# Optimization experiments

Hardware: AMD Instinct MI355X
Metric: run time of the kernel (lower is better)

The kernel has to match this reference:

```python
import jax, jax.numpy as jnp
import numpy as np

B, T, D, H = 4, 2048, 1024, 16
HD = D // H  # head dim = 64


def setup_inputs() -> dict:
    key = jax.random.key(0)
    ks = jax.random.split(key, 6)
    s = 0.02
    return {
        "x": jax.random.normal(ks[0], (B, T, D), dtype=jnp.float32),
        "Wk": jax.random.normal(ks[1], (D, D), dtype=jnp.float32) * s,
        "Wq": jax.random.normal(ks[2], (D, D), dtype=jnp.float32) * s,
        "Wv": jax.random.normal(ks[3], (D, D), dtype=jnp.float32) * s,
        "Wp": jax.random.normal(ks[4], (D, D), dtype=jnp.float32) * s,
        "bp": jnp.zeros((D,), dtype=jnp.float32),
    }


def reference(x, Wk, Wq, Wv, Wp, bp):
    # nn.Linear applies x @ W.T; weights here are stored torch-style [out, in]
    Bq, Tq, _ = x.shape
    k = (x @ Wk.T).reshape(Bq, Tq, H, HD).transpose(0, 2, 1, 3)  # [B,H,T,hd]
    q = (x @ Wq.T).reshape(Bq, Tq, H, HD).transpose(0, 2, 1, 3)
    v = (x @ Wv.T).reshape(Bq, Tq, H, HD).transpose(0, 2, 1, 3)
    scale = HD ** -0.5
    attn = jnp.einsum('bhqd,bhkd->bhqk', q, k) * scale  # [B,H,T,T]
    causal = jnp.tril(jnp.ones((Tq, Tq), dtype=bool))
    attn = jnp.where(causal, attn, -jnp.inf)
    attn = jax.nn.softmax(attn, axis=-1)
    # dropout p=0.0 -> identity (eval semantics)
    out = jnp.einsum('bhqk,bhkd->bhqd', attn, v)  # [B,H,T,hd]
    out = out.transpose(0, 2, 1, 3).reshape(Bq, Tq, D)
    return out @ Wp.T + bp
```

## Files before the change

### kernel.cpp

```cpp
#include <hip/hip_runtime.h>
#include <hip/hip_bf16.h>
#include <stdint.h>


typedef __bf16 bf16x8 __attribute__((ext_vector_type(8)));
typedef float floatx4 __attribute__((ext_vector_type(4)));
typedef unsigned short ushort_t;
typedef unsigned short ushortx8 __attribute__((ext_vector_type(8)));
typedef unsigned short ushortx4 __attribute__((ext_vector_type(4)));
typedef short shortx4 __attribute__((ext_vector_type(4)));

#define MFMA16(a, b, c) __builtin_amdgcn_mfma_f32_16x16x32_bf16((a), (b), (c), 0, 0, 0)
#define MFMA16K16(a, b, c) __builtin_amdgcn_mfma_f32_16x16x16bf16_1k((a), (b), (c), 0, 0, 0)
#define EXP2F(x) __builtin_amdgcn_exp2f(x)

static __device__ __forceinline__ ushort_t f2bfu(float f) {
  union { float f; unsigned u; } v; v.f = f;
  unsigned r = v.u + 0x7FFFu + ((v.u >> 16) & 1u);
  return (ushort_t)(r >> 16);
}

static __device__ __forceinline__ unsigned pack_bf2(float lo, float hi) {
  return __builtin_amdgcn_perm(__float_as_uint(hi), __float_as_uint(lo), 0x07060302);
}

static __device__ __forceinline__ void gl_lds16(const void* g, void* l) {
  __builtin_amdgcn_global_load_lds(
      (const __attribute__((address_space(1))) void*)g,
      (__attribute__((address_space(3))) void*)l, 16, 0, 0);
}

__global__ void cvt_all(const float* __restrict__ x,  const float* __restrict__ wk,
                        const float* __restrict__ wq, const float* __restrict__ wv,
                        const float* __restrict__ wp, ushortx4* __restrict__ dst) {
  const int i = blockIdx.x * blockDim.x + threadIdx.x;
  const float4* src; int off;
  if (i < 2097152) { src = (const float4*)x; off = i; }
  else {
    const int r = i - 2097152;
    const int sel = r >> 18;
    off = r & 262143;
    src = (const float4*)(sel == 0 ? wk : sel == 1 ? wq : sel == 2 ? wv : wp);
  }
  const float4 f = src[off];
  ushortx4 o;
  o[0] = f2bfu(f.x); o[1] = f2bfu(f.y); o[2] = f2bfu(f.z); o[3] = f2bfu(f.w);
  dst[i] = o;
}

__global__ __launch_bounds__(512, 2) void gemm_qkv(
    const ushort_t* __restrict__ X,
    const ushort_t* __restrict__ Wq, const ushort_t* __restrict__ Wk,
    const ushort_t* __restrict__ Wv,
    ushort_t* __restrict__ qb, ushort_t* __restrict__ kb, ushort_t* __restrict__ vtb)
{
  const int L = (int)blockIdx.x;
  const int rr = L & 7, mm = L >> 3;
  const int m0 = (rr + 8 * (mm & 3)) * 256;
  const int rest = mm >> 2;
  const int n0 = (rest & 3) * 256;
  const int z = rest >> 2;

  const ushort_t* Bm = (z == 0) ? Wq : (z == 1) ? Wk : Wv;

  __shared__ ushort_t As0[256 * 64];
  __shared__ ushort_t As1[256 * 64];
  __shared__ ushort_t Bs0[256 * 64];
  __shared__ ushort_t Bs1[256 * 64];

  const int tid = threadIdx.x;
  const int w = tid >> 6, lane = tid & 63, g = lane >> 4, c = lane & 15;
  const int wm = w >> 2, wn = w & 3;
  const int cswz = c & 7;

  floatx4 acc[8][4];
  const floatx4 zero4 = {0.f, 0.f, 0.f, 0.f};
#pragma unroll
  for (int i = 0; i < 8; ++i)
#pragma unroll
    for (int j = 0; j < 4; ++j) acc[i][j] = zero4;

  const int srow = tid >> 3;
  const int gsw  = ((tid & 7) ^ (srow & 7)) * 8;

#pragma unroll
  for (int p = 0; p < 4; ++p) {
    gl_lds16(&X [(size_t)(m0 + p * 64 + srow) * 1024 + gsw], &As0[p * 4096 + tid * 8]);
    gl_lds16(&Bm[(size_t)(n0 + p * 64 + srow) * 1024 + gsw], &Bs0[p * 4096 + tid * 8]);
  }

  auto ktile = [&](const ushort_t* __restrict__ Ac, const ushort_t* __restrict__ Bc,
                   ushort_t* __restrict__ An, ushort_t* __restrict__ Bn,
                   int kn, bool stagenext) {
    if (stagenext) {
      gl_lds16(&X [(size_t)(m0 + srow) * 1024 + kn + gsw], &An[tid * 8]);
      gl_lds16(&Bm[(size_t)(n0 + srow) * 1024 + kn + gsw], &Bn[tid * 8]);
      asm volatile("s_waitcnt vmcnt(2)" ::: "memory");
    } else {
      asm volatile("s_waitcnt vmcnt(0)" ::: "memory");
    }
    __builtin_amdgcn_s_barrier();

    bf16x8 bfr[4][2];
#pragma unroll
    for (int j = 0; j < 4; ++j)
#pragma unroll
      for (int kk = 0; kk < 2; ++kk)
        bfr[j][kk] = *reinterpret_cast<const bf16x8*>(
            &Bc[(wn * 64 + j * 16 + c) * 64 + ((kk * 4 + g) ^ cswz) * 8]);

#pragma unroll
    for (int q = 0; q < 4; ++q) {
      bf16x8 af[2][2];
#pragma unroll
      for (int ii = 0; ii < 2; ++ii)
#pragma unroll
        for (int kk = 0; kk < 2; ++kk)
          af[ii][kk] = *reinterpret_cast<const bf16x8*>(
              &Ac[(wm * 128 + (q * 2 + ii) * 16 + c) * 64 + ((kk * 4 + g) ^ cswz) * 8]);
      if (q && stagenext) {
        gl_lds16(&X [(size_t)(m0 + q * 64 + srow) * 1024 + kn + gsw], &An[q * 4096 + tid * 8]);
        gl_lds16(&Bm[(size_t)(n0 + q * 64 + srow) * 1024 + kn + gsw], &Bn[q * 4096 + tid * 8]);
      }
      __builtin_amdgcn_s_setprio(1);
#pragma unroll
      for (int ii = 0; ii < 2; ++ii)
#pragma unroll
        for (int j = 0; j < 4; ++j)
#pragma unroll
          for (int kk = 0; kk < 2; ++kk)
            acc[q * 2 + ii][j] = MFMA16(af[ii][kk], bfr[j][kk], acc[q * 2 + ii][j]);
      __builtin_amdgcn_s_setprio(0);
    }
    __builtin_amdgcn_s_barrier();
  };

  for (int kt = 0; kt < 16; kt += 2) {
    ktile(As0, Bs0, As1, Bs1, (kt + 1) * 64, true);
    ktile(As1, Bs1, As0, Bs0, (kt + 2) * 64, kt < 14);
  }

#pragma unroll
  for (int i = 0; i < 8; ++i) {
#pragma unroll
    for (int j = 0; j < 4; ++j) {
      const int mbase = m0 + wm * 128 + i * 16 + g * 4;
      const int n = n0 + wn * 64 + j * 16 + c;
      const int h = n >> 6, d = n & 63;
      if (z == 2) {
        const int bb = mbase >> 11, t = mbase & 2047;
        ushortx4 pk;
#pragma unroll
        for (int r = 0; r < 4; ++r) pk[r] = f2bfu(acc[i][j][r]);
        *reinterpret_cast<ushortx4*>(&vtb[(size_t)((bb * 16 + h) * 64 + d) * 2048 + t]) = pk;
      } else {
        ushort_t* ob = (z == 0) ? qb : kb;
#pragma unroll
        for (int r = 0; r < 4; ++r) {
          const int m = mbase + r;
          const int bb = m >> 11, t = m & 2047;
          ob[(size_t)((bb * 16 + h) * 2048 + t) * 64 + d] = f2bfu(acc[i][j][r]);
        }
      }
    }
  }
}

__global__ __launch_bounds__(256, 4) void attn_kernel(
    const ushort_t* __restrict__ qbuf, const ushort_t* __restrict__ kbuf,
    const ushort_t* __restrict__ vtbuf, ushort_t* __restrict__ obuf)
{
  const int L = (int)(blockIdx.x + 16 * (blockIdx.y + 16 * blockIdx.z));
  const int rr = L & 7, mm = L >> 3;
  const int j = mm >> 3;
  const int bhl = rr * 8 + (mm & 7);
  const int h = bhl & 15, b = bhl >> 4;

  const int tid = threadIdx.x, w = tid >> 6, lane = tid & 63, g = lane >> 4, c = lane & 15;

  __shared__ ushort_t Kl[128 * 64];
  __shared__ ushort_t Vl[64 * 128];

  const size_t bh = (size_t)(b * 16 + h);
  const ushort_t* kb_bh = kbuf + bh * 2048 * 64;
  const ushort_t* vt_bh = vtbuf + bh * 64 * 2048;
  const ushort_t* qb_bh = qbuf + bh * 2048 * 64;

  const int rb0 = j * 64 + w * 16;
  const int rb1 = (31 - j) * 64 + w * 16;

  bf16x8 aq0[2], aq1[2];
  {
    const ushort_t* qp0 = qb_bh + (size_t)(rb0 + c) * 64;
    aq0[0] = *reinterpret_cast<const bf16x8*>(qp0 + g * 8);
    aq0[1] = *reinterpret_cast<const bf16x8*>(qp0 + 32 + g * 8);
    const ushort_t* qp1 = qb_bh + (size_t)(rb1 + c) * 64;
    aq1[0] = *reinterpret_cast<const bf16x8*>(qp1 + g * 8);
    aq1[1] = *reinterpret_cast<const bf16x8*>(qp1 + 32 + g * 8);
  }

  floatx4 oacc0[4], oacc1[4];
  float l0 = 0.f, l1 = 0.f;
  const floatx4 zero4 = {0.f, 0.f, 0.f, 0.f};
#pragma unroll
  for (int td = 0; td < 4; ++td) { oacc0[td] = zero4; oacc1[td] = zero4; }

  const int krow_s = tid >> 3;
  const int kgsw   = ((tid & 7) ^ (krow_s & 7)) * 8;
  const int vrow_s = tid >> 4;
  const int vgsw   = ((tid & 15) ^ (vrow_s & 15)) * 8;

  const float SCALE = 0.18033688011112042f;

  const int n128 = (33 - j) >> 1;
  for (int kt = 0; kt < n128; ++kt) {
    const int key0 = kt * 128;
#pragma unroll
    for (int p = 0; p < 4; ++p) {
      const int kr = p * 32 + krow_s;
      gl_lds16(&kb_bh[(size_t)(key0 + kr) * 64 + kgsw], &Kl[p * 2048 + tid * 8]);
      const int vr = p * 16 + vrow_s;
      gl_lds16(&vt_bh[(size_t)vr * 2048 + key0 + vgsw], &Vl[p * 2048 + tid * 8]);
    }
    __syncthreads();

#pragma unroll
    for (int s = 0; s < 2; ++s) {
      const int ti = 2 * kt + s;
      const int key0s = ti * 64;
#pragma unroll
      for (int grp = 0; grp < 2; ++grp) {
        const int lim = (grp == 0) ? j : 31 - j;
        if (ti > lim) continue;
        const int rb = (grp == 0) ? rb0 : rb1;
        const bf16x8 b0 = (grp == 0) ? aq0[0] : aq1[0];
        const bf16x8 b1 = (grp == 0) ? aq0[1] : aq1[1];

        float pv[4][4];
#pragma unroll
        for (int t4 = 0; t4 < 4; ++t4) {
          const int krow = s * 64 + t4 * 16 + c;
          const bf16x8 k0f = *reinterpret_cast<const bf16x8*>(&Kl[krow * 64 + ((g) ^ (c & 7)) * 8]);
          const bf16x8 k1f = *reinterpret_cast<const bf16x8*>(&Kl[krow * 64 + ((4 + g) ^ (c & 7)) * 8]);
          floatx4 sa = zero4;
          sa = MFMA16(k0f, b0, sa);
          sa = MFMA16(k1f, b1, sa);
          if (ti == lim) {
            const int q = rb + c;
#pragma unroll
            for (int r = 0; r < 4; ++r) {
              const int key = key0s + t4 * 16 + g * 4 + r;
              const float e = EXP2F(sa[r] * SCALE);
              pv[t4][r] = (key <= q) ? e : 0.f;
            }
          } else {
#pragma unroll
            for (int r = 0; r < 4; ++r) pv[t4][r] = EXP2F(sa[r] * SCALE);
          }
        }
        float lsum = 0.f;
#pragma unroll
        for (int t4 = 0; t4 < 4; ++t4)
          lsum += (pv[t4][0] + pv[t4][1]) + (pv[t4][2] + pv[t4][3]);
        if (grp == 0) l0 += lsum; else l1 += lsum;

#pragma unroll
        for (int t4 = 0; t4 < 4; ++t4) {
          union { unsigned u[2]; shortx4 v; } pk;
          pk.u[0] = pack_bf2(pv[t4][0], pv[t4][1]);
          pk.u[1] = pack_bf2(pv[t4][2], pv[t4][3]);
          const int cc = s * 8 + t4 * 2 + (g >> 1);
          const int ko = (g & 1) * 4;
#pragma unroll
          for (int td = 0; td < 4; ++td) {
            const shortx4 va = *reinterpret_cast<const shortx4*>(
                &Vl[(td * 16 + c) * 128 + (cc ^ c) * 8 + ko]);
            if (grp == 0) oacc0[td] = MFMA16K16(va, pk.v, oacc0[td]);
            else          oacc1[td] = MFMA16K16(va, pk.v, oacc1[td]);
          }
        }
      }
    }
    __syncthreads();
  }

#pragma unroll
  for (int grp = 0; grp < 2; ++grp) {
    float ls = (grp == 0) ? l0 : l1;
    ls += __shfl_xor(ls, 16, 64);
    ls += __shfl_xor(ls, 32, 64);
    const float inv = 1.f / ls;
    const int q = ((grp == 0) ? rb0 : rb1) + c;
    ushort_t* ob = &obuf[((size_t)(b * 2048 + q) * 16 + h) * 64];
#pragma unroll
    for (int td = 0; td < 4; ++td) {
      const floatx4 oa = (grp == 0) ? oacc0[td] : oacc1[td];
      ushortx4 pk;
#pragma unroll
      for (int r = 0; r < 4; ++r) pk[r] = f2bfu(oa[r] * inv);
      *reinterpret_cast<ushortx4*>(&ob[td * 16 + g * 4]) = pk;
    }
  }
}

__global__ __launch_bounds__(256) void gemm_proj(
    const ushort_t* __restrict__ A, const ushort_t* __restrict__ Wp,
    const float* __restrict__ bias, float* __restrict__ out)
{
  const int L = (int)(blockIdx.x + 64 * blockIdx.y);
  const int rr = L & 7, mm = L >> 3;
  const int m0 = (rr + 8 * (mm & 7)) * 128;
  const int n0 = (mm >> 3) * 128;

  __shared__ ushort_t Al[128 * 64];
  __shared__ ushort_t Bl[128 * 64];
  const int tid = threadIdx.x;
  const int w = tid >> 6, lane = tid & 63, g = lane >> 4, c = lane & 15;
  const int wm = w >> 1, wn = w & 1;
  const int cswz = c & 7;

  floatx4 acc[4][4];
  const floatx4 zero4 = {0.f, 0.f, 0.f, 0.f};
#pragma unroll
  for (int i = 0; i < 4; ++i)
#pragma unroll
    for (int j = 0; j < 4; ++j) acc[i][j] = zero4;

  const int srow = tid >> 3;
  const int gsw  = ((tid & 7) ^ (srow & 7)) * 8;

  for (int k0 = 0; k0 < 1024; k0 += 64) {
#pragma unroll
    for (int p = 0; p < 4; ++p) {
      const int row = p * 32 + srow;
      gl_lds16(&A [(size_t)(m0 + row) * 1024 + k0 + gsw], &Al[p * 2048 + tid * 8]);
      gl_lds16(&Wp[(size_t)(n0 + row) * 1024 + k0 + gsw], &Bl[p * 2048 + tid * 8]);
    }
    __syncthreads();
#pragma unroll
    for (int kk = 0; kk < 2; ++kk) {
      bf16x8 af[4], bfr[4];
#pragma unroll
      for (int i = 0; i < 4; ++i) {
        const int sw = ((kk * 4 + g) ^ cswz) * 8;
        af[i]  = *reinterpret_cast<const bf16x8*>(&Al[(wm * 64 + i * 16 + c) * 64 + sw]);
        bfr[i] = *reinterpret_cast<const bf16x8*>(&Bl[(wn * 64 + i * 16 + c) * 64 + sw]);
      }
#pragma unroll
      for (int i = 0; i < 4; ++i)
#pragma unroll
        for (int j = 0; j < 4; ++j)
          acc[i][j] = MFMA16(af[i], bfr[j], acc[i][j]);
    }
    __syncthreads();
  }

#pragma unroll
  for (int i = 0; i < 4; ++i) {
#pragma unroll
    for (int j = 0; j < 4; ++j) {
      const int n = n0 + wn * 64 + j * 16 + c;
      const float bv = bias[n];
#pragma unroll
      for (int r = 0; r < 4; ++r) {
        const int m = m0 + wm * 64 + i * 16 + g * 4 + r;
        out[(size_t)m * 1024 + n] = acc[i][j][r] + bv;
      }
    }
  }
}

extern "C" void kernel_launch(void* const* d_in, const int* in_sizes, int n_in,
                              void* d_out, int out_size, void* d_ws, size_t ws_size,
                              hipStream_t stream) {
  const float* x  = (const float*)d_in[0];
  const float* Wk = (const float*)d_in[1];
  const float* Wq = (const float*)d_in[2];
  const float* Wv = (const float*)d_in[3];
  const float* Wp = (const float*)d_in[4];
  const float* bp = (const float*)d_in[5];
  float* out = (float*)d_out;

  char* ws = (char*)d_ws;
  const size_t SZ_X = (size_t)8192 * 1024 * 2;
  const size_t SZ_W = (size_t)1024 * 1024 * 2;
  ushort_t* xb    = (ushort_t*)ws;  ws += SZ_X;
  ushort_t* wkb   = (ushort_t*)ws;  ws += SZ_W;
  ushort_t* wqb   = (ushort_t*)ws;  ws += SZ_W;
  ushort_t* wvb   = (ushort_t*)ws;  ws += SZ_W;
  ushort_t* wpb   = (ushort_t*)ws;  ws += SZ_W;
  ushort_t* qbuf  = (ushort_t*)ws;  ws += SZ_X;
  ushort_t* kbuf  = (ushort_t*)ws;  ws += SZ_X;
  ushort_t* vtbuf = (ushort_t*)ws;  ws += SZ_X;
  ushort_t* obuf  = xb;

  cvt_all<<<12288, 256, 0, stream>>>(x, Wk, Wq, Wv, Wp, (ushortx4*)xb);

  gemm_qkv<<<dim3(384), 512, 0, stream>>>(xb, wqb, wkb, wvb, qbuf, kbuf, vtbuf);
  attn_kernel<<<dim3(16, 16, 4), 256, 0, stream>>>(qbuf, kbuf, vtbuf, obuf);
  gemm_proj<<<dim3(64, 8), 256, 0, stream>>>(obuf, wpb, bp, out);
}
```

Before: 240.4 us.

## Shrink QKV GEMM tile to 256x128 and pipeline projection GEMM

The QKV GEMM tile drops from 256x256 to 256x128, which doubles the grid to 768 blocks and halves the per-thread accumulators. Staging of the next k-tile is split into two halves placed around an intra-tile barrier. The projection GEMM is rewritten to use the same double-buffered, 512-thread, 256x128-tile pipeline with async global-to-LDS loads, replacing its single-buffered 128x128 loop. The aim is better occupancy and load balance across CUs and overlap of loads with MFMA work in the projection, at the cost of lower operand reuse per block in the QKV GEMM.

```diff
diff --git a/kernel.cpp b/kernel.cpp
--- a/kernel.cpp
+++ b/kernel.cpp
@@ -58,25 +58,25 @@
   const int rr = L & 7, mm = L >> 3;
   const int m0 = (rr + 8 * (mm & 3)) * 256;
   const int rest = mm >> 2;
-  const int n0 = (rest & 3) * 256;
-  const int z = rest >> 2;
+  const int n0 = (rest & 7) * 128;
+  const int z = rest >> 3;
 
   const ushort_t* Bm = (z == 0) ? Wq : (z == 1) ? Wk : Wv;
 
   __shared__ ushort_t As0[256 * 64];
   __shared__ ushort_t As1[256 * 64];
-  __shared__ ushort_t Bs0[256 * 64];
-  __shared__ ushort_t Bs1[256 * 64];
+  __shared__ ushort_t Bs0[128 * 64];
+  __shared__ ushort_t Bs1[128 * 64];
 
   const int tid = threadIdx.x;
   const int w = tid >> 6, lane = tid & 63, g = lane >> 4, c = lane & 15;
-  const int wm = w >> 2, wn = w & 3;
+  const int wm = w >> 1, wn = w & 1;
   const int cswz = c & 7;
 
-  floatx4 acc[8][4];
+  floatx4 acc[4][4];
   const floatx4 zero4 = {0.f, 0.f, 0.f, 0.f};
 #pragma unroll
-  for (int i = 0; i < 8; ++i)
+  for (int i = 0; i < 4; ++i)
 #pragma unroll
     for (int j = 0; j < 4; ++j) acc[i][j] = zero4;
 
@@ -84,18 +84,19 @@
   const int gsw  = ((tid & 7) ^ (srow & 7)) * 8;
 
 #pragma unroll
-  for (int p = 0; p < 4; ++p) {
+  for (int p = 0; p < 4; ++p)
     gl_lds16(&X [(size_t)(m0 + p * 64 + srow) * 1024 + gsw], &As0[p * 4096 + tid * 8]);
+#pragma unroll
+  for (int p = 0; p < 2; ++p)
     gl_lds16(&Bm[(size_t)(n0 + p * 64 + srow) * 1024 + gsw], &Bs0[p * 4096 + tid * 8]);
-  }
-
-  auto ktile = [&](const ushort_t* __restrict__ Ac, const ushort_t* __restrict__ Bc,
-                   ushort_t* __restrict__ An, ushort_t* __restrict__ Bn,
-                   int kn, bool stagenext) {
+
+  auto ktile = [&](const ushort_t* Ac, const ushort_t* Bc,
+                   ushort_t* An, ushort_t* Bn, int kn, bool stagenext) {
     if (stagenext) {
-      gl_lds16(&X [(size_t)(m0 + srow) * 1024 + kn + gsw], &An[tid * 8]);
-      gl_lds16(&Bm[(size_t)(n0 + srow) * 1024 + kn + gsw], &Bn[tid * 8]);
-      asm volatile("s_waitcnt vmcnt(2)" ::: "memory");
+      gl_lds16(&X [(size_t)(m0 +       srow) * 1024 + kn + gsw], &An[           tid * 8]);
+      gl_lds16(&X [(size_t)(m0 +  64 + srow) * 1024 + kn + gsw], &An[    4096 + tid * 8]);
+      gl_lds16(&Bm[(size_t)(n0 +       srow) * 1024 + kn + gsw], &Bn[           tid * 8]);
+      asm volatile("s_waitcnt vmcnt(3)" ::: "memory");
     } else {
       asm volatile("s_waitcnt vmcnt(0)" ::: "memory");
     }
@@ -109,29 +110,46 @@
         bfr[j][kk] = *reinterpret_cast<const bf16x8*>(
             &Bc[(wn * 64 + j * 16 + c) * 64 + ((kk * 4 + g) ^ cswz) * 8]);
 
-#pragma unroll
-    for (int q = 0; q < 4; ++q) {
-      bf16x8 af[2][2];
-#pragma unroll
-      for (int ii = 0; ii < 2; ++ii)
+    bf16x8 af[2][2];
+#pragma unroll
+    for (int ii = 0; ii < 2; ++ii)
+#pragma unroll
+      for (int kk = 0; kk < 2; ++kk)
+        af[ii][kk] = *reinterpret_cast<const bf16x8*>(
+            &Ac[(wm * 64 + ii * 16 + c) * 64 + ((kk * 4 + g) ^ cswz) * 8]);
+
+    __builtin_amdgcn_s_setprio(1);
+#pragma unroll
+    for (int ii = 0; ii < 2; ++ii)
+#pragma unroll
+      for (int j = 0; j < 4; ++j)
 #pragma unroll
         for (int kk = 0; kk < 2; ++kk)
-          af[ii][kk] = *reinterpret_cast<const bf16x8*>(
-              &Ac[(wm * 128 + (q * 2 + ii) * 16 + c) * 64 + ((kk * 4 + g) ^ cswz) * 8]);
-      if (q && stagenext) {
-        gl_lds16(&X [(size_t)(m0 + q * 64 + srow) * 1024 + kn + gsw], &An[q * 4096 + tid * 8]);
-        gl_lds16(&Bm[(size_t)(n0 + q * 64 + srow) * 1024 + kn + gsw], &Bn[q * 4096 + tid * 8]);
-      }
-      __builtin_amdgcn_s_setprio(1);
-#pragma unroll
-      for (int ii = 0; ii < 2; ++ii)
-#pragma unroll
-        for (int j = 0; j < 4; ++j)
-#pragma unroll
-          for (int kk = 0; kk < 2; ++kk)
-            acc[q * 2 + ii][j] = MFMA16(af[ii][kk], bfr[j][kk], acc[q * 2 + ii][j]);
-      __builtin_amdgcn_s_setprio(0);
-    }
+          acc[ii][j] = MFMA16(af[ii][kk], bfr[j][kk], acc[ii][j]);
+    __builtin_amdgcn_s_setprio(0);
+    __builtin_amdgcn_s_barrier();
+
+    if (stagenext) {
+      gl_lds16(&X [(size_t)(m0 + 128 + srow) * 1024 + kn + gsw], &An[2 * 4096 + tid * 8]);
+      gl_lds16(&X [(size_t)(m0 + 192 + srow) * 1024 + kn + gsw], &An[3 * 4096 + tid * 8]);
+      gl_lds16(&Bm[(size_t)(n0 +  64 + srow) * 1024 + kn + gsw], &Bn[    4096 + tid * 8]);
+    }
+#pragma unroll
+    for (int ii = 0; ii < 2; ++ii)
+#pragma unroll
+      for (int kk = 0; kk < 2; ++kk)
+        af[ii][kk] = *reinterpret_cast<const bf16x8*>(
+            &Ac[(wm * 64 + (2 + ii) * 16 + c) * 64 + ((kk * 4 + g) ^ cswz) * 8]);
+
+    __builtin_amdgcn_s_setprio(1);
+#pragma unroll
+    for (int ii = 0; ii < 2; ++ii)
+#pragma unroll
+      for (int j = 0; j < 4; ++j)
+#pragma unroll
+        for (int kk = 0; kk < 2; ++kk)
+          acc[2 + ii][j] = MFMA16(af[ii][kk], bfr[j][kk], acc[2 + ii][j]);
+    __builtin_amdgcn_s_setprio(0);
     __builtin_amdgcn_s_barrier();
   };
 
@@ -141,10 +159,10 @@
   }
 
 #pragma unroll
-  for (int i = 0; i < 8; ++i) {
+  for (int i = 0; i < 4; ++i) {
 #pragma unroll
     for (int j = 0; j < 4; ++j) {
-      const int mbase = m0 + wm * 128 + i * 16 + g * 4;
+      const int mbase = m0 + wm * 64 + i * 16 + g * 4;
       const int n = n0 + wn * 64 + j * 16 + c;
       const int h = n >> 6, d = n & 63;
       if (z == 2) {
@@ -303,17 +321,20 @@
   }
 }
 
-__global__ __launch_bounds__(256) void gemm_proj(
+__global__ __launch_bounds__(512, 2) void gemm_proj(
     const ushort_t* __restrict__ A, const ushort_t* __restrict__ Wp,
     const float* __restrict__ bias, float* __restrict__ out)
 {
-  const int L = (int)(blockIdx.x + 64 * blockIdx.y);
+  const int L = (int)blockIdx.x;
   const int rr = L & 7, mm = L >> 3;
-  const int m0 = (rr + 8 * (mm & 7)) * 128;
-  const int n0 = (mm >> 3) * 128;
-
-  __shared__ ushort_t Al[128 * 64];
-  __shared__ ushort_t Bl[128 * 64];
+  const int m0 = (rr + 8 * (mm & 3)) * 256;
+  const int n0 = (mm >> 2) * 128;
+
+  __shared__ ushort_t As0[256 * 64];
+  __shared__ ushort_t As1[256 * 64];
+  __shared__ ushort_t Bs0[128 * 64];
+  __shared__ ushort_t Bs1[128 * 64];
+
   const int tid = threadIdx.x;
   const int w = tid >> 6, lane = tid & 63, g = lane >> 4, c = lane & 15;
   const int wm = w >> 1, wn = w & 1;
@@ -329,30 +350,79 @@
   const int srow = tid >> 3;
   const int gsw  = ((tid & 7) ^ (srow & 7)) * 8;
 
-  for (int k0 = 0; k0 < 1024; k0 += 64) {
-#pragma unroll
-    for (int p = 0; p < 4; ++p) {
-      const int row = p * 32 + srow;
-      gl_lds16(&A [(size_t)(m0 + row) * 1024 + k0 + gsw], &Al[p * 2048 + tid * 8]);
-      gl_lds16(&Wp[(size_t)(n0 + row) * 1024 + k0 + gsw], &Bl[p * 2048 + tid * 8]);
-    }
-    __syncthreads();
-#pragma unroll
-    for (int kk = 0; kk < 2; ++kk) {
-      bf16x8 af[4], bfr[4];
-#pragma unroll
-      for (int i = 0; i < 4; ++i) {
-        const int sw = ((kk * 4 + g) ^ cswz) * 8;
-        af[i]  = *reinterpret_cast<const bf16x8*>(&Al[(wm * 64 + i * 16 + c) * 64 + sw]);
-        bfr[i] = *reinterpret_cast<const bf16x8*>(&Bl[(wn * 64 + i * 16 + c) * 64 + sw]);
-      }
-#pragma unroll
-      for (int i = 0; i < 4; ++i)
-#pragma unroll
-        for (int j = 0; j < 4; ++j)
-          acc[i][j] = MFMA16(af[i], bfr[j], acc[i][j]);
-    }
-    __syncthreads();
+#pragma unroll
+  for (int p = 0; p < 4; ++p)
+    gl_lds16(&A [(size_t)(m0 + p * 64 + srow) * 1024 + gsw], &As0[p * 4096 + tid * 8]);
+#pragma unroll
+  for (int p = 0; p < 2; ++p)
+    gl_lds16(&Wp[(size_t)(n0 + p * 64 + srow) * 1024 + gsw], &Bs0[p * 4096 + tid * 8]);
+
+  auto ktile = [&](const ushort_t* Ac, const ushort_t* Bc,
+                   ushort_t* An, ushort_t* Bn, int kn, bool stagenext) {
+    if (stagenext) {
+      gl_lds16(&A [(size_t)(m0 +       srow) * 1024 + kn + gsw], &An[           tid * 8]);
+      gl_lds16(&A [(size_t)(m0 +  64 + srow) * 1024 + kn + gsw], &An[    4096 + tid * 8]);
+      gl_lds16(&Wp[(size_t)(n0 +       srow) * 1024 + kn + gsw], &Bn[           tid * 8]);
+      asm volatile("s_waitcnt vmcnt(3)" ::: "memory");
+    } else {
+      asm volatile("s_waitcnt vmcnt(0)" ::: "memory");
+    }
+    __builtin_amdgcn_s_barrier();
+
+    bf16x8 bfr[4][2];
+#pragma unroll
+    for (int j = 0; j < 4; ++j)
+#pragma unroll
+      for (int kk = 0; kk < 2; ++kk)
+        bfr[j][kk] = *reinterpret_cast<const bf16x8*>(
+            &Bc[(wn * 64 + j * 16 + c) * 64 + ((kk * 4 + g) ^ cswz) * 8]);
+
+    bf16x8 af[2][2];
+#pragma unroll
+    for (int ii = 0; ii < 2; ++ii)
+#pragma unroll
+      for (int kk = 0; kk < 2; ++kk)
+        af[ii][kk] = *reinterpret_cast<const bf16x8*>(
+            &Ac[(wm * 64 + ii * 16 + c) * 64 + ((kk * 4 + g) ^ cswz) * 8]);
+
+    __builtin_amdgcn_s_setprio(1);
+#pragma unroll
+    for (int ii = 0; ii < 2; ++ii)
+#pragma unroll
+      for (int j = 0; j < 4; ++j)
+#pragma unroll
+        for (int kk = 0; kk < 2; ++kk)
+          acc[ii][j] = MFMA16(af[ii][kk], bfr[j][kk], acc[ii][j]);
+    __builtin_amdgcn_s_setprio(0);
+    __builtin_amdgcn_s_barrier();
+
+    if (stagenext) {
+      gl_lds16(&A [(size_t)(m0 + 128 + srow) * 1024 + kn + gsw], &An[2 * 4096 + tid * 8]);
+      gl_lds16(&A [(size_t)(m0 + 192 + srow) * 1024 + kn + gsw], &An[3 * 4096 + tid * 8]);
+      gl_lds16(&Wp[(size_t)(n0 +  64 + srow) * 1024 + kn + gsw], &Bn[    4096 + tid * 8]);
+    }
+#pragma unroll
+    for (int ii = 0; ii < 2; ++ii)
+#pragma unroll
+      for (int kk = 0; kk < 2; ++kk)
+        af[ii][kk] = *reinterpret_cast<const bf16x8*>(
+            &Ac[(wm * 64 + (2 + ii) * 16 + c) * 64 + ((kk * 4 + g) ^ cswz) * 8]);
+
+    __builtin_amdgcn_s_setprio(1);
+#pragma unroll
+    for (int ii = 0; ii < 2; ++ii)
+#pragma unroll
+      for (int j = 0; j < 4; ++j)
+#pragma unroll
+        for (int kk = 0; kk < 2; ++kk)
+          acc[2 + ii][j] = MFMA16(af[ii][kk], bfr[j][kk], acc[2 + ii][j]);
+    __builtin_amdgcn_s_setprio(0);
+    __builtin_amdgcn_s_barrier();
+  };
+
+  for (int kt = 0; kt < 16; kt += 2) {
+    ktile(As0, Bs0, As1, Bs1, (kt + 1) * 64, true);
+    ktile(As1, Bs1, As0, Bs0, (kt + 2) * 64, kt < 14);
   }
 
 #pragma unroll
@@ -396,7 +466,7 @@
 
   cvt_all<<<12288, 256, 0, stream>>>(x, Wk, Wq, Wv, Wp, (ushortx4*)xb);
 
-  gemm_qkv<<<dim3(384), 512, 0, stream>>>(xb, wqb, wkb, wvb, qbuf, kbuf, vtbuf);
+  gemm_qkv<<<dim3(768), 512, 0, stream>>>(xb, wqb, wkb, wvb, qbuf, kbuf, vtbuf);
   attn_kernel<<<dim3(16, 16, 4), 256, 0, stream>>>(qbuf, kbuf, vtbuf, obuf);
-  gemm_proj<<<dim3(64, 8), 256, 0, stream>>>(obuf, wpb, bp, out);
-}
+  gemm_proj<<<dim3(256), 512, 0, stream>>>(obuf, wpb, bp, out);
+}
```

New measurement: 241.9 us. No clear change (+0.6%).
